# Optimization experiments

Measured on AMD Instinct MI355X. Metric: run time of the kernel, lower is better.

## Reference

```python
import jax, jax.numpy as jnp
import numpy as np

C = 1024
RANK = 8


def _layernorm(x, g, b, eps=1e-5):
    mu = jnp.mean(x, axis=-1, keepdims=True)
    var = jnp.var(x, axis=-1, keepdims=True)
    return (x - mu) * jax.lax.rsqrt(var + eps) * g + b


def setup_inputs() -> dict:
    key = jax.random.key(0)
    ks = jax.random.split(key, 10)
    B, T = 4, 4096
    x = jax.random.normal(ks[0], (B, T, C), dtype=jnp.float32)
    # parameters (match torch inits)
    W0 = jnp.eye(C, dtype=jnp.float32) * 0.1
    A_init = jax.random.normal(ks[1], (C, RANK), dtype=jnp.float32) * 0.01
    B_init = jnp.zeros((RANK, C), dtype=jnp.float32)
    log_lr = jnp.full((C,), float(np.log(0.1)), dtype=jnp.float32)
    s = 1.0 / np.sqrt(C)
    Wq = jax.random.uniform(ks[2], (C, C), minval=-s, maxval=s, dtype=jnp.float32)
    Wk = jax.random.uniform(ks[3], (C, C), minval=-s, maxval=s, dtype=jnp.float32)
    Wv = jax.random.uniform(ks[4], (C, C), minval=-s, maxval=s, dtype=jnp.float32)
    Wo = jax.random.uniform(ks[5], (C, C), minval=-s, maxval=s, dtype=jnp.float32)
    Wg = jax.random.uniform(ks[6], (C, C), minval=-s, maxval=s, dtype=jnp.float32)
    ln_g = jnp.ones((C,), dtype=jnp.float32)
    ln_b = jnp.zeros((C,), dtype=jnp.float32)
    ls_g = jnp.full((C,), 1e-4, dtype=jnp.float32)  # LayerScale gamma
    return {"x": x, "W0": W0, "A_init": A_init, "B_init": B_init,
            "log_lr": log_lr, "Wq": Wq, "Wk": Wk, "Wv": Wv, "Wo": Wo,
            "Wg": Wg, "ln_g": ln_g, "ln_b": ln_b, "ls_g": ls_g}


def reference(x, W0, A_init, B_init, log_lr, Wq, Wk, Wv, Wo, Wg, ln_g, ln_b, ls_g):
    B, T, _ = x.shape
    h = _layernorm(x, ln_g, ln_b)
    # dual-form TTT (training path: q/k/v projections, full K @ W0)
    Q = jnp.einsum('btc,dc->btd', h, Wq)
    K = jnp.einsum('btc,dc->btd', h, Wk)
    V = jnp.einsum('btc,dc->btd', h, Wv)
    lr = jnp.minimum(jnp.exp(log_lr), 1.0)  # clamp(max=1.0)
    y0 = jnp.einsum('btc,cd->btd', K, W0) + jnp.einsum('btr,rd->btd', jnp.einsum('btc,cr->btr', K, A_init), B_init)
    error = y0 - V
    loss = jnp.mean(error ** 2)
    gradient = K * error                     # [B,T,C]
    grad_cumsum = jnp.cumsum(gradient, axis=1)
    grad_shift = jnp.concatenate([jnp.zeros((B, 1, gradient.shape[-1]), gradient.dtype), grad_cumsum[:, :-1, :]], axis=1)
    correction = Q * lr[None, None, :] * grad_shift
    pos = jnp.arange(1, T + 1, dtype=correction.dtype)
    pos_scale = (1.0 / (1.0 + 0.1 * jnp.log(pos)))[None, :, None]
    out = y0 - correction * pos_scale
    # gate, out projection, layer scale, residual
    gate = jax.nn.sigmoid(jnp.einsum('btc,dc->btd', x, Wg))
    out = out * gate
    out = jnp.einsum('btc,dc->btd', out, Wo) * ls_g
    return (x + out, loss)
```

## Files before the change

kernel.cpp:

```cpp
#include <hip/hip_runtime.h>
#include <stdint.h>
#include <math.h>

typedef unsigned short u16;
typedef __attribute__((ext_vector_type(8))) short short8;
typedef __attribute__((ext_vector_type(4))) float f32x4;

__device__ __forceinline__ float bf2f(u16 u){
  union { unsigned int i; float f; } v; v.i = ((unsigned int)u) << 16; return v.f;
}
__device__ __forceinline__ u16 f2bf(float f){
  union { float f; unsigned int i; } v; v.f = f;
  return (u16)((v.i + 0x7FFFu + ((v.i >> 16) & 1u)) >> 16);
}

__global__ void ln_prep(const float* __restrict__ x, const float* __restrict__ g,
                        const float* __restrict__ bta, u16* __restrict__ h,
                        u16* __restrict__ xb, float* __restrict__ loss){
  if (blockIdx.x == 0 && threadIdx.x == 0) loss[0] = 0.f;
  int row = blockIdx.x, tid = threadIdx.x;
  const float4* xr = (const float4*)(x + (size_t)row * 1024);
  float4 v = xr[tid];
  float s  = v.x + v.y + v.z + v.w;
  float s2 = v.x*v.x + v.y*v.y + v.z*v.z + v.w*v.w;
  #pragma unroll
  for (int o = 32; o > 0; o >>= 1){ s += __shfl_down(s, o); s2 += __shfl_down(s2, o); }
  __shared__ float red[8];
  if ((tid & 63) == 0){ red[tid >> 6] = s; red[4 + (tid >> 6)] = s2; }
  __syncthreads();
  float ts = red[0]+red[1]+red[2]+red[3];
  float t2 = red[4]+red[5]+red[6]+red[7];
  float mu   = ts * (1.0f/1024.0f);
  float var  = t2 * (1.0f/1024.0f) - mu*mu;
  float rstd = rsqrtf(var + 1e-5f);
  float4 gg = ((const float4*)g)[tid];
  float4 bb = ((const float4*)bta)[tid];
  ushort4 hv, xv;
  hv.x = f2bf((v.x-mu)*rstd*gg.x + bb.x);
  hv.y = f2bf((v.y-mu)*rstd*gg.y + bb.y);
  hv.z = f2bf((v.z-mu)*rstd*gg.z + bb.z);
  hv.w = f2bf((v.w-mu)*rstd*gg.w + bb.w);
  xv.x = f2bf(v.x); xv.y = f2bf(v.y); xv.z = f2bf(v.z); xv.w = f2bf(v.w);
  ((ushort4*)h )[(size_t)row*256 + tid] = hv;
  ((ushort4*)xb)[(size_t)row*256 + tid] = xv;
}

__global__ void conv5(const float* __restrict__ a, const float* __restrict__ b,
                      const float* __restrict__ c, const float* __restrict__ d,
                      const float* __restrict__ e,
                      u16* oa, u16* ob, u16* oc, u16* od, u16* oe){
  int sel = blockIdx.y;
  const float* s = sel==0?a : sel==1?b : sel==2?c : sel==3?d : e;
  u16* o = sel==0?oa : sel==1?ob : sel==2?oc : sel==3?od : oe;
  int i = blockIdx.x*256 + threadIdx.x;
  float4 v = ((const float4*)s)[i];
  ushort4 r; r.x=f2bf(v.x); r.y=f2bf(v.y); r.z=f2bf(v.z); r.w=f2bf(v.w);
  ((ushort4*)o)[i] = r;
}

__global__ void weff_k(const float* __restrict__ W0, const float* __restrict__ Ai,
                       const float* __restrict__ Bi, u16* __restrict__ Wet){
  __shared__ float tile[32][33];
  int d0 = blockIdx.x*32, e0 = blockIdx.y*32;
  int tid = threadIdx.x;
  int lr = tid >> 5, lc = tid & 31;
  #pragma unroll
  for (int s = 0; s < 4; ++s){
    int e = e0 + s*8 + lr, d = d0 + lc;
    float v = W0[(size_t)e*1024 + d];
    #pragma unroll
    for (int r = 0; r < 8; ++r) v += Ai[e*8 + r] * Bi[(size_t)r*1024 + d];
    tile[s*8 + lr][lc] = v;
  }
  __syncthreads();
  #pragma unroll
  for (int s = 0; s < 4; ++s){
    int d = d0 + s*8 + lr, e = e0 + lc;
    Wet[(size_t)d*1024 + e] = f2bf(tile[lc][s*8 + lr]);
  }
}

template<int EPI>
__device__ __forceinline__ void gemm_body(const u16* __restrict__ A, const u16* __restrict__ Bm,
    u16* __restrict__ Cb, float* __restrict__ Cf, const float* __restrict__ lsg,
    const float* __restrict__ xres,
    const u16* __restrict__ Kb2, const u16* __restrict__ Vb2,
    u16* __restrict__ Gr, float* __restrict__ part, float* __restrict__ loss,
    int mblk, int nblk){
  __shared__ u16 As[128*64];
  __shared__ u16 Bs[128*64];
  const int tid  = threadIdx.x;
  const int lane = tid & 63;
  const int w    = tid >> 6;
  const int m0 = mblk * 128, n0 = nblk * 128;
  const int lrow = lane >> 3;
  const int gcol8 = (((lane & 7) ^ (lrow & 7)) * 8);
  const int wm = w & 1, wn = w >> 1;
  const int l15 = lane & 15, quad = lane >> 4;
  const int sw  = (l15 & 7);

  f32x4 acc[4][4] = {};

  #pragma unroll 1
  for (int kk = 0; kk < 1024; kk += 64){
    #pragma unroll
    for (int it = 0; it < 4; ++it){
      int r0 = w*8 + it*32;
      const u16* ga = A  + (size_t)(m0 + r0 + lrow)*1024 + kk + gcol8;
      __builtin_amdgcn_global_load_lds((const __attribute__((address_space(1))) unsigned int*)ga,
          (__attribute__((address_space(3))) unsigned int*)(As + r0*64), 16, 0, 0);
      const u16* gb = Bm + (size_t)(n0 + r0 + lrow)*1024 + kk + gcol8;
      __builtin_amdgcn_global_load_lds((const __attribute__((address_space(1))) unsigned int*)gb,
          (__attribute__((address_space(3))) unsigned int*)(Bs + r0*64), 16, 0, 0);
    }
    __syncthreads();
    #pragma unroll
    for (int kh = 0; kh < 2; ++kh){
      int kbi = kh*4 + quad;
      int koff = ((kbi ^ sw) * 8);
      short8 af[4], bfv[4];
      #pragma unroll
      for (int i = 0; i < 4; ++i) af[i]  = *(const short8*)(As + (wm*64 + i*16 + l15)*64 + koff);
      #pragma unroll
      for (int j = 0; j < 4; ++j) bfv[j] = *(const short8*)(Bs + (wn*64 + j*16 + l15)*64 + koff);
      #pragma unroll
      for (int i = 0; i < 4; ++i)
        #pragma unroll
        for (int j = 0; j < 4; ++j)
          acc[i][j] = __builtin_amdgcn_mfma_f32_16x16x32_bf16(af[i], bfv[j], acc[i][j], 0, 0, 0);
    }
    __syncthreads();
  }

  const int rbase = quad * 4;
  if (EPI == 0){
    #pragma unroll
    for (int i = 0; i < 4; ++i){
      int row = m0 + wm*64 + i*16 + rbase;
      #pragma unroll
      for (int j = 0; j < 4; ++j){
        int col = n0 + wn*64 + j*16 + l15;
        #pragma unroll
        for (int r = 0; r < 4; ++r)
          Cb[(size_t)(row + r)*1024 + col] = f2bf(acc[i][j][r]);
      }
    }
  } else if (EPI == 1){
    float lsv[4];
    #pragma unroll
    for (int j = 0; j < 4; ++j) lsv[j] = lsg[n0 + wn*64 + j*16 + l15];
    #pragma unroll
    for (int i = 0; i < 4; ++i){
      int row = m0 + wm*64 + i*16 + rbase;
      #pragma unroll
      for (int j = 0; j < 4; ++j){
        int col = n0 + wn*64 + j*16 + l15;
        #pragma unroll
        for (int r = 0; r < 4; ++r){
          size_t idx = (size_t)(row + r)*1024 + col;
          Cf[idx] = acc[i][j][r] * lsv[j] + xres[idx];
        }
      }
    }
  } else {
    float csum[4] = {0.f, 0.f, 0.f, 0.f};
    float ls = 0.f;
    #pragma unroll
    for (int i = 0; i < 4; ++i){
      int row = m0 + wm*64 + i*16 + rbase;
      #pragma unroll
      for (int j = 0; j < 4; ++j){
        int col = n0 + wn*64 + j*16 + l15;
        #pragma unroll
        for (int r = 0; r < 4; ++r){
          size_t idx = (size_t)(row + r)*1024 + col;
          float y  = acc[i][j][r];
          float kv = bf2f(Kb2[idx]);
          float vv = bf2f(Vb2[idx]);
          float e  = y - vv;
          float gv = kv * e;
          Cb[idx] = f2bf(y);
          Gr[idx] = f2bf(gv);
          csum[j] += gv;
          ls += e * e;
        }
      }
    }
    float* colred = (float*)As;
    if (tid < 132) colred[tid] = 0.f;
    __syncthreads();
    #pragma unroll
    for (int j = 0; j < 4; ++j) atomicAdd(&colred[wn*64 + j*16 + l15], csum[j]);
    #pragma unroll
    for (int o = 32; o > 0; o >>= 1) ls += __shfl_down(ls, o);
    if (lane == 0) atomicAdd(&colred[128 + w], ls);
    __syncthreads();
    if (tid < 128) part[(size_t)mblk * 1024 + n0 + tid] = colred[tid];
    if (tid == 0) atomicAdd(loss, colred[128]+colred[129]+colred[130]+colred[131]);
  }
}

__global__ void gemm_qkvg(const u16* __restrict__ h, const u16* __restrict__ xb,
                          const u16* __restrict__ Wqb, const u16* __restrict__ Wkb,
                          const u16* __restrict__ Wvb, const u16* __restrict__ Wgb,
                          u16* __restrict__ Qb, u16* __restrict__ Kb,
                          u16* __restrict__ Vb, u16* __restrict__ Gb){
  int sel = blockIdx.y >> 3;
  const u16* A  = (sel == 3) ? xb : h;
  const u16* Bm = sel==0?Wqb : sel==1?Wkb : sel==2?Wvb : Wgb;
  u16* Out      = sel==0?Qb  : sel==1?Kb  : sel==2?Vb  : Gb;
  gemm_body<0>(A, Bm, Out, nullptr, nullptr, nullptr,
               nullptr, nullptr, nullptr, nullptr, nullptr, blockIdx.x, blockIdx.y & 7);
}

__global__ void gemm_y0(const u16* __restrict__ Kb, const u16* __restrict__ Wet,
                        u16* __restrict__ Yb, const u16* __restrict__ Vb,
                        u16* __restrict__ Gr, float* __restrict__ part,
                        float* __restrict__ loss){
  gemm_body<2>(Kb, Wet, Yb, nullptr, nullptr, nullptr,
               Kb, Vb, Gr, part, loss, blockIdx.x, blockIdx.y);
}

__global__ void gemm_final(const u16* __restrict__ A, const u16* __restrict__ Bm,
                           float* __restrict__ C, const float* __restrict__ lsg,
                           const float* __restrict__ xres){
  gemm_body<1>(A, Bm, nullptr, C, lsg, xres,
               nullptr, nullptr, nullptr, nullptr, nullptr, blockIdx.x, blockIdx.y);
}

__global__ void scan2(const u16* __restrict__ Gr, const u16* __restrict__ Yb,
                      const u16* __restrict__ Qb, const u16* __restrict__ Gb,
                      const float* __restrict__ part, const float* __restrict__ llr,
                      u16* __restrict__ OutPre){
  int tid = threadIdx.x;
  int c = blockIdx.x*256 + tid;
  int ch = blockIdx.y, b = blockIdx.z;
  float run = 0.f;
  for (int j = 0; j < ch; ++j) run += part[((size_t)(b*32 + j))*1024 + c];
  float lrc = fminf(expf(llr[c]), 1.0f);
  size_t base = ((size_t)b*4096 + (size_t)ch*128)*1024 + c;
  #pragma unroll 4
  for (int t = 0; t < 128; ++t){
    size_t idx = base + (size_t)t*1024;
    float gr = bf2f(Gr[idx]);
    float yv = bf2f(Yb[idx]);
    float qv = bf2f(Qb[idx]);
    float gl = bf2f(Gb[idx]);
    int tg = ch*128 + t + 1;
    float ps = 1.0f/(1.0f + 0.1f*logf((float)tg));
    float gate = 1.0f/(1.0f + expf(-gl));
    float o = (yv - qv*lrc*run*ps) * gate;
    OutPre[idx] = f2bf(o);
    run += gr;
  }
}

__global__ void finloss(const float* __restrict__ loss, float* __restrict__ o){
  o[0] = loss[0] * (1.0f/16777216.0f);
}

extern "C" void kernel_launch(void* const* d_in, const int* in_sizes, int n_in,
                              void* d_out, int out_size, void* d_ws, size_t ws_size,
                              hipStream_t stream){
  const float* x   = (const float*)d_in[0];
  const float* W0  = (const float*)d_in[1];
  const float* Ai  = (const float*)d_in[2];
  const float* Bi  = (const float*)d_in[3];
  const float* llr = (const float*)d_in[4];
  const float* Wq  = (const float*)d_in[5];
  const float* Wk  = (const float*)d_in[6];
  const float* Wv  = (const float*)d_in[7];
  const float* Wo  = (const float*)d_in[8];
  const float* Wg  = (const float*)d_in[9];
  const float* lng = (const float*)d_in[10];
  const float* lnb = (const float*)d_in[11];
  const float* lsg = (const float*)d_in[12];
  float* out = (float*)d_out;

  const size_t TOK = 16384, CC = 1024;
  char* p = (char*)d_ws;
  float* loss = (float*)p; p += 256;
  u16* h   = (u16*)p; p += TOK*CC*2;
  u16* xb  = (u16*)p; p += TOK*CC*2;
  u16* Qb  = (u16*)p; p += TOK*CC*2;
  u16* Kb  = (u16*)p; p += TOK*CC*2;
  u16* Vb  = (u16*)p; p += TOK*CC*2;
  u16* Gb  = (u16*)p; p += TOK*CC*2;
  u16* Wqb = (u16*)p; p += CC*CC*2;
  u16* Wkb = (u16*)p; p += CC*CC*2;
  u16* Wvb = (u16*)p; p += CC*CC*2;
  u16* Wgb = (u16*)p; p += CC*CC*2;
  u16* Wob = (u16*)p; p += CC*CC*2;
  u16* Wet = (u16*)p; p += CC*CC*2;
  float* part = (float*)p; p += (size_t)128*1024*4;

  ln_prep<<<16384, 256, 0, stream>>>(x, lng, lnb, h, xb, loss);
  conv5<<<dim3(1024, 5), 256, 0, stream>>>(Wq, Wk, Wv, Wg, Wo, Wqb, Wkb, Wvb, Wgb, Wob);
  weff_k<<<dim3(32, 32), 256, 0, stream>>>(W0, Ai, Bi, Wet);
  gemm_qkvg<<<dim3(128, 32), 256, 0, stream>>>(h, xb, Wqb, Wkb, Wvb, Wgb, Qb, Kb, Vb, Gb);
  gemm_y0<<<dim3(128, 8), 256, 0, stream>>>(Kb, Wet, h, Vb, xb, part, loss);
  scan2<<<dim3(4, 32, 4), 256, 0, stream>>>(xb, h, Qb, Gb, part, llr, Qb);
  gemm_final<<<dim3(128, 8), 256, 0, stream>>>(Qb, Wob, out, lsg, x);
  finloss<<<1, 1, 0, stream>>>(loss, out + 16777216);
}
```

Baseline: 500.6 us.

## Fuse y0 GEMM with chunked cumsum scan via decoupled lookback chaining

Merges the y0 GEMM epilogue and the separate scan kernel into one kernel. Blocks take ordered tickets, compute the per-chunk column sums of the gradient, and chain inclusive prefixes across time chunks through flags in global memory. Each block then does a local column scan in LDS and writes the gated output directly, so the Y and gradient tensors no longer round-trip through memory. The final GEMM epilogue is also restaged through LDS to get coalesced float4 stores and residual loads, and position scales and learning rates are precomputed in a small kernel. The trade-off is serial dependence between chunks of the same chain, plus spin-wait overhead.

```diff
diff --git a/kernel.cpp b/kernel.cpp
--- a/kernel.cpp
+++ b/kernel.cpp
@@ -80,15 +80,22 @@
   }
 }
 
+__global__ void psk2(const float* __restrict__ llr, float* __restrict__ psg,
+                     float* __restrict__ lrc, unsigned* __restrict__ flags,
+                     unsigned* __restrict__ ticket){
+  int t = blockIdx.x*256 + threadIdx.x;
+  psg[t] = 1.0f/(1.0f + 0.1f*logf((float)(t+1)));
+  if (t < 1024){ lrc[t] = fminf(expf(llr[t]), 1.0f); flags[t] = 0u; }
+  if (t == 0) *ticket = 0u;
+}
+
 template<int EPI>
 __device__ __forceinline__ void gemm_body(const u16* __restrict__ A, const u16* __restrict__ Bm,
     u16* __restrict__ Cb, float* __restrict__ Cf, const float* __restrict__ lsg,
-    const float* __restrict__ xres,
-    const u16* __restrict__ Kb2, const u16* __restrict__ Vb2,
-    u16* __restrict__ Gr, float* __restrict__ part, float* __restrict__ loss,
-    int mblk, int nblk){
-  __shared__ u16 As[128*64];
-  __shared__ u16 Bs[128*64];
+    const float* __restrict__ xres, int mblk, int nblk){
+  __shared__ u16 smem[16384];
+  u16* As = smem;
+  u16* Bs = smem + 8192;
   const int tid  = threadIdx.x;
   const int lane = tid & 63;
   const int w    = tid >> 6;
@@ -145,58 +152,33 @@
           Cb[(size_t)(row + r)*1024 + col] = f2bf(acc[i][j][r]);
       }
     }
-  } else if (EPI == 1){
-    float lsv[4];
-    #pragma unroll
-    for (int j = 0; j < 4; ++j) lsv[j] = lsg[n0 + wn*64 + j*16 + l15];
+  } else {
+    float* cf = (float*)smem;
+    const int lr = tid >> 3, seg = tid & 7;
+    float4 lsv[4];
+    #pragma unroll
+    for (int k = 0; k < 4; ++k) lsv[k] = *(const float4*)(lsg + n0 + seg*16 + k*4);
     #pragma unroll
     for (int i = 0; i < 4; ++i){
-      int row = m0 + wm*64 + i*16 + rbase;
-      #pragma unroll
-      for (int j = 0; j < 4; ++j){
-        int col = n0 + wn*64 + j*16 + l15;
+      __syncthreads();
+      #pragma unroll
+      for (int j = 0; j < 4; ++j)
         #pragma unroll
-        for (int r = 0; r < 4; ++r){
-          size_t idx = (size_t)(row + r)*1024 + col;
-          Cf[idx] = acc[i][j][r] * lsv[j] + xres[idx];
-        }
+        for (int r = 0; r < 4; ++r)
+          cf[(wm*16 + rbase + r)*132 + wn*64 + j*16 + l15] = acc[i][j][r];
+      __syncthreads();
+      int grow = m0 + i*16 + (lr & 15) + (lr >> 4)*64;
+      size_t gbase = (size_t)grow*1024 + n0 + seg*16;
+      #pragma unroll
+      for (int k = 0; k < 4; ++k){
+        float4 o = *(const float4*)(cf + lr*132 + seg*16 + k*4);
+        float4 xr = *(const float4*)(xres + gbase + k*4);
+        float4 res;
+        res.x = o.x*lsv[k].x + xr.x; res.y = o.y*lsv[k].y + xr.y;
+        res.z = o.z*lsv[k].z + xr.z; res.w = o.w*lsv[k].w + xr.w;
+        *(float4*)(Cf + gbase + k*4) = res;
       }
     }
-  } else {
-    float csum[4] = {0.f, 0.f, 0.f, 0.f};
-    float ls = 0.f;
-    #pragma unroll
-    for (int i = 0; i < 4; ++i){
-      int row = m0 + wm*64 + i*16 + rbase;
-      #pragma unroll
-      for (int j = 0; j < 4; ++j){
-        int col = n0 + wn*64 + j*16 + l15;
-        #pragma unroll
-        for (int r = 0; r < 4; ++r){
-          size_t idx = (size_t)(row + r)*1024 + col;
-          float y  = acc[i][j][r];
-          float kv = bf2f(Kb2[idx]);
-          float vv = bf2f(Vb2[idx]);
-          float e  = y - vv;
-          float gv = kv * e;
-          Cb[idx] = f2bf(y);
-          Gr[idx] = f2bf(gv);
-          csum[j] += gv;
-          ls += e * e;
-        }
-      }
-    }
-    float* colred = (float*)As;
-    if (tid < 132) colred[tid] = 0.f;
-    __syncthreads();
-    #pragma unroll
-    for (int j = 0; j < 4; ++j) atomicAdd(&colred[wn*64 + j*16 + l15], csum[j]);
-    #pragma unroll
-    for (int o = 32; o > 0; o >>= 1) ls += __shfl_down(ls, o);
-    if (lane == 0) atomicAdd(&colred[128 + w], ls);
-    __syncthreads();
-    if (tid < 128) part[(size_t)mblk * 1024 + n0 + tid] = colred[tid];
-    if (tid == 0) atomicAdd(loss, colred[128]+colred[129]+colred[130]+colred[131]);
   }
 }
 
@@ -209,50 +191,165 @@
   const u16* A  = (sel == 3) ? xb : h;
   const u16* Bm = sel==0?Wqb : sel==1?Wkb : sel==2?Wvb : Wgb;
   u16* Out      = sel==0?Qb  : sel==1?Kb  : sel==2?Vb  : Gb;
-  gemm_body<0>(A, Bm, Out, nullptr, nullptr, nullptr,
-               nullptr, nullptr, nullptr, nullptr, nullptr, blockIdx.x, blockIdx.y & 7);
-}
-
-__global__ void gemm_y0(const u16* __restrict__ Kb, const u16* __restrict__ Wet,
-                        u16* __restrict__ Yb, const u16* __restrict__ Vb,
-                        u16* __restrict__ Gr, float* __restrict__ part,
-                        float* __restrict__ loss){
-  gemm_body<2>(Kb, Wet, Yb, nullptr, nullptr, nullptr,
-               Kb, Vb, Gr, part, loss, blockIdx.x, blockIdx.y);
+  gemm_body<0>(A, Bm, Out, nullptr, nullptr, nullptr, blockIdx.x, blockIdx.y & 7);
 }
 
 __global__ void gemm_final(const u16* __restrict__ A, const u16* __restrict__ Bm,
                            float* __restrict__ C, const float* __restrict__ lsg,
                            const float* __restrict__ xres){
-  gemm_body<1>(A, Bm, nullptr, C, lsg, xres,
-               nullptr, nullptr, nullptr, nullptr, nullptr, blockIdx.x, blockIdx.y);
-}
-
-__global__ void scan2(const u16* __restrict__ Gr, const u16* __restrict__ Yb,
-                      const u16* __restrict__ Qb, const u16* __restrict__ Gb,
-                      const float* __restrict__ part, const float* __restrict__ llr,
-                      u16* __restrict__ OutPre){
-  int tid = threadIdx.x;
-  int c = blockIdx.x*256 + tid;
-  int ch = blockIdx.y, b = blockIdx.z;
-  float run = 0.f;
-  for (int j = 0; j < ch; ++j) run += part[((size_t)(b*32 + j))*1024 + c];
-  float lrc = fminf(expf(llr[c]), 1.0f);
-  size_t base = ((size_t)b*4096 + (size_t)ch*128)*1024 + c;
-  #pragma unroll 4
-  for (int t = 0; t < 128; ++t){
-    size_t idx = base + (size_t)t*1024;
-    float gr = bf2f(Gr[idx]);
-    float yv = bf2f(Yb[idx]);
-    float qv = bf2f(Qb[idx]);
-    float gl = bf2f(Gb[idx]);
-    int tg = ch*128 + t + 1;
-    float ps = 1.0f/(1.0f + 0.1f*logf((float)tg));
-    float gate = 1.0f/(1.0f + expf(-gl));
-    float o = (yv - qv*lrc*run*ps) * gate;
-    OutPre[idx] = f2bf(o);
-    run += gr;
-  }
+  gemm_body<1>(A, Bm, nullptr, C, lsg, xres, blockIdx.x, blockIdx.y);
+}
+
+__global__ void gemm_y0_scan(const u16* __restrict__ Kb, const u16* __restrict__ Wet,
+                             const u16* __restrict__ Vb, const u16* Qb,
+                             const u16* __restrict__ Gb,
+                             const float* __restrict__ lrc, const float* __restrict__ psg,
+                             u16* OutPre, float* __restrict__ Incl,
+                             unsigned* __restrict__ flags, unsigned* __restrict__ ticket,
+                             float* __restrict__ loss){
+  __shared__ u16 smem[17424];
+  u16* As = smem;
+  u16* Bs = smem + 8192;
+  __shared__ unsigned tk_s;
+  const int tid  = threadIdx.x;
+  const int lane = tid & 63;
+  const int w    = tid >> 6;
+  if (tid == 0) tk_s = atomicAdd(ticket, 1u);
+  __syncthreads();
+  const unsigned tk = tk_s;
+  const int ch = tk >> 5, sub = tk & 31;
+  const int chain = sub;
+  const int b = sub >> 3, nblk = sub & 7;
+  const int mblk = b*32 + ch;
+  const int m0 = mblk * 128, n0 = nblk * 128;
+  const int lrow = lane >> 3;
+  const int gcol8 = (((lane & 7) ^ (lrow & 7)) * 8);
+  const int wm = w & 1, wn = w >> 1;
+  const int l15 = lane & 15, quad = lane >> 4;
+  const int sw  = (l15 & 7);
+
+  f32x4 acc[4][4] = {};
+
+  #pragma unroll 1
+  for (int kk = 0; kk < 1024; kk += 64){
+    #pragma unroll
+    for (int it = 0; it < 4; ++it){
+      int r0 = w*8 + it*32;
+      const u16* ga = Kb  + (size_t)(m0 + r0 + lrow)*1024 + kk + gcol8;
+      __builtin_amdgcn_global_load_lds((const __attribute__((address_space(1))) unsigned int*)ga,
+          (__attribute__((address_space(3))) unsigned int*)(As + r0*64), 16, 0, 0);
+      const u16* gb = Wet + (size_t)(n0 + r0 + lrow)*1024 + kk + gcol8;
+      __builtin_amdgcn_global_load_lds((const __attribute__((address_space(1))) unsigned int*)gb,
+          (__attribute__((address_space(3))) unsigned int*)(Bs + r0*64), 16, 0, 0);
+    }
+    __syncthreads();
+    #pragma unroll
+    for (int kh = 0; kh < 2; ++kh){
+      int kbi = kh*4 + quad;
+      int koff = ((kbi ^ sw) * 8);
+      short8 af[4], bfv[4];
+      #pragma unroll
+      for (int i = 0; i < 4; ++i) af[i]  = *(const short8*)(As + (wm*64 + i*16 + l15)*64 + koff);
+      #pragma unroll
+      for (int j = 0; j < 4; ++j) bfv[j] = *(const short8*)(Bs + (wn*64 + j*16 + l15)*64 + koff);
+      #pragma unroll
+      for (int i = 0; i < 4; ++i)
+        #pragma unroll
+        for (int j = 0; j < 4; ++j)
+          acc[i][j] = __builtin_amdgcn_mfma_f32_16x16x32_bf16(af[i], bfv[j], acc[i][j], 0, 0, 0);
+    }
+    __syncthreads();
+  }
+
+  const int rbase = quad * 4;
+  u16*  gvt  = smem;
+  float* aggf = (float*)(smem + 16896);
+
+  float csum[4] = {0.f, 0.f, 0.f, 0.f};
+  float ls = 0.f;
+  #pragma unroll
+  for (int i = 0; i < 4; ++i){
+    int rowl = wm*64 + i*16 + rbase;
+    #pragma unroll
+    for (int j = 0; j < 4; ++j){
+      int coll = wn*64 + j*16 + l15;
+      #pragma unroll
+      for (int r = 0; r < 4; ++r){
+        size_t idx = (size_t)(m0 + rowl + r)*1024 + n0 + coll;
+        float y  = acc[i][j][r];
+        float kv = bf2f(Kb[idx]);
+        float vv = bf2f(Vb[idx]);
+        float e  = y - vv;
+        float gv = kv * e;
+        ls += e*e;
+        csum[j] += gv;
+        gvt[(rowl + r)*132 + coll] = f2bf(gv);
+      }
+    }
+  }
+  #pragma unroll
+  for (int j = 0; j < 4; ++j){
+    csum[j] += __shfl_xor(csum[j], 16);
+    csum[j] += __shfl_xor(csum[j], 32);
+  }
+  if (quad == 0){
+    #pragma unroll
+    for (int j = 0; j < 4; ++j) aggf[wm*128 + wn*64 + j*16 + l15] = csum[j];
+  }
+  #pragma unroll
+  for (int o = 32; o > 0; o >>= 1) ls += __shfl_down(ls, o);
+  if (lane == 0) aggf[256 + w] = ls;
+  __syncthreads();
+
+  float P = 0.f;
+  if (tid < 128){
+    float aggc = aggf[tid] + aggf[128 + tid];
+    if (ch > 0){
+      const unsigned fi = chain*32 + ch - 1;
+      while (__hip_atomic_load(&flags[fi], __ATOMIC_ACQUIRE, __HIP_MEMORY_SCOPE_AGENT) == 0u)
+        __builtin_amdgcn_s_sleep(8);
+      P = __hip_atomic_load(&Incl[(size_t)fi*128 + tid], __ATOMIC_RELAXED, __HIP_MEMORY_SCOPE_AGENT);
+    }
+    __hip_atomic_store(&Incl[((size_t)chain*32 + ch)*128 + tid], P + aggc,
+                       __ATOMIC_RELAXED, __HIP_MEMORY_SCOPE_AGENT);
+  }
+  __syncthreads();
+  if (tid == 0)
+    __hip_atomic_store(&flags[chain*32 + ch], 1u, __ATOMIC_RELEASE, __HIP_MEMORY_SCOPE_AGENT);
+
+  if (tid < 128){
+    float run = P;
+    u16* colp = gvt + tid;
+    #pragma unroll 4
+    for (int t = 0; t < 128; ++t){
+      float g = bf2f(colp[t*132]);
+      colp[t*132] = f2bf(run);
+      run += g;
+    }
+  }
+  __syncthreads();
+
+  #pragma unroll
+  for (int i = 0; i < 4; ++i){
+    int rowl = wm*64 + i*16 + rbase;
+    #pragma unroll
+    for (int j = 0; j < 4; ++j){
+      int coll = wn*64 + j*16 + l15;
+      float lrcv = lrc[n0 + coll];
+      #pragma unroll
+      for (int r = 0; r < 4; ++r){
+        size_t idx = (size_t)(m0 + rowl + r)*1024 + n0 + coll;
+        float run = bf2f(gvt[(rowl + r)*132 + coll]);
+        float ps  = psg[ch*128 + rowl + r];
+        float q   = bf2f(Qb[idx]);
+        float gl  = bf2f(Gb[idx]);
+        float gate = 1.0f/(1.0f + expf(-gl));
+        float o = (acc[i][j][r] - q*lrcv*run*ps) * gate;
+        OutPre[idx] = f2bf(o);
+      }
+    }
+  }
+  if (tid == 0) atomicAdd(loss, aggf[256]+aggf[257]+aggf[258]+aggf[259]);
 }
 
 __global__ void finloss(const float* __restrict__ loss, float* __restrict__ o){
@@ -292,14 +389,19 @@
   u16* Wgb = (u16*)p; p += CC*CC*2;
   u16* Wob = (u16*)p; p += CC*CC*2;
   u16* Wet = (u16*)p; p += CC*CC*2;
-  float* part = (float*)p; p += (size_t)128*1024*4;
+  float*    psg    = (float*)p;    p += 4096*4;
+  float*    lrc    = (float*)p;    p += 1024*4;
+  float*    Incl   = (float*)p;    p += (size_t)1024*128*4;
+  unsigned* flags  = (unsigned*)p; p += 1024*4;
+  unsigned* ticket = (unsigned*)p; p += 256;
 
   ln_prep<<<16384, 256, 0, stream>>>(x, lng, lnb, h, xb, loss);
   conv5<<<dim3(1024, 5), 256, 0, stream>>>(Wq, Wk, Wv, Wg, Wo, Wqb, Wkb, Wvb, Wgb, Wob);
   weff_k<<<dim3(32, 32), 256, 0, stream>>>(W0, Ai, Bi, Wet);
+  psk2<<<16, 256, 0, stream>>>(llr, psg, lrc, flags, ticket);
   gemm_qkvg<<<dim3(128, 32), 256, 0, stream>>>(h, xb, Wqb, Wkb, Wvb, Wgb, Qb, Kb, Vb, Gb);
-  gemm_y0<<<dim3(128, 8), 256, 0, stream>>>(Kb, Wet, h, Vb, xb, part, loss);
-  scan2<<<dim3(4, 32, 4), 256, 0, stream>>>(xb, h, Qb, Gb, part, llr, Qb);
+  gemm_y0_scan<<<1024, 256, 0, stream>>>(Kb, Wet, Vb, Qb, Gb, lrc, psg, Qb,
+                                         Incl, flags, ticket, loss);
   gemm_final<<<dim3(128, 8), 256, 0, stream>>>(Qb, Wob, out, lsg, x);
   finloss<<<1, 1, 0, stream>>>(loss, out + 16777216);
 }
```

After: 1.244 ms. 149% more time.
